# Kernel tuning notes

Measured on AMD Instinct MI355X. Metric: run time of the kernel, lower is better.

The kernel has to match this reference:

```python
import jax, jax.numpy as jnp
from jax import lax
import numpy as np

B, T = 512, 64
VOCAB, EMB, HID, NIMG = 10000, 512, 1024, 2048


def setup_inputs() -> dict:
    key = jax.random.key(0)
    ks = jax.random.split(key, 8)
    s_ih = 1.0 / np.sqrt(HID)
    return {
        "m": jax.random.randint(ks[0], (B, T), 0, VOCAB),
        "emb": jax.random.normal(ks[1], (VOCAB, EMB), dtype=jnp.float32),
        "W_ih": jax.random.uniform(ks[2], (4 * HID, EMB), minval=-s_ih, maxval=s_ih, dtype=jnp.float32),
        "W_hh": jax.random.uniform(ks[3], (4 * HID, HID), minval=-s_ih, maxval=s_ih, dtype=jnp.float32),
        "b_ih": jax.random.uniform(ks[4], (4 * HID,), minval=-s_ih, maxval=s_ih, dtype=jnp.float32),
        "b_hh": jax.random.uniform(ks[5], (4 * HID,), minval=-s_ih, maxval=s_ih, dtype=jnp.float32),
        "W_out": jax.random.normal(ks[6], (NIMG, HID), dtype=jnp.float32) * (1.0 / np.sqrt(HID)),
        "b_out": jnp.zeros((NIMG,), dtype=jnp.float32),
    }


def reference(m, emb, W_ih, W_hh, b_ih, b_hh, W_out, b_out):
    # m: [B, T] int tokens. Embed all steps at once, scan over time.
    x = emb[m]                      # [B, T, E]
    x = jnp.swapaxes(x, 0, 1)       # [T, B, E] (matches m.permute(1,0) step order)
    Bsz = m.shape[0]
    H = W_hh.shape[1]
    h0 = jnp.zeros((Bsz, H), dtype=emb.dtype)
    c0 = jnp.zeros((Bsz, H), dtype=emb.dtype)

    def step(carry, xt):
        h, c = carry
        # PyTorch LSTMCell gate order: input, forget, cell(g), output
        gates = xt @ W_ih.T + b_ih + h @ W_hh.T + b_hh  # [B, 4H]
        i, f, g, o = jnp.split(gates, 4, axis=-1)
        i = jax.nn.sigmoid(i)
        f = jax.nn.sigmoid(f)
        g = jnp.tanh(g)
        o = jax.nn.sigmoid(o)
        c = f * c + i * g
        h = o * jnp.tanh(c)
        return (h, c), None

    (h, _), _ = lax.scan(step, (h0, c0), x)
    return h @ W_out.T + b_out      # [B, n_image_features]
```

## Files before the change

kernel.cpp:

```cpp
#include <hip/hip_runtime.h>
#include <cstdint>

#define B_    512
#define T_    64
#define VOCAB_ 10000
#define VPAD_ 10112
#define EMB_  512
#define HID_  1024
#define G4H_  4096
#define KCAT_ 1536
#define NIMG_ 2048

typedef _Float16 half8 __attribute__((ext_vector_type(8)));
typedef _Float16 half4 __attribute__((ext_vector_type(4)));
typedef float floatx4 __attribute__((ext_vector_type(4)));

__device__ __forceinline__ void async_copy16(void* lds_uniform, const void* gsrc) {
    __builtin_amdgcn_global_load_lds(
        (__attribute__((address_space(1))) void*)(uintptr_t)gsrc,
        (__attribute__((address_space(3))) void*)(uint32_t)(uintptr_t)lds_uniform,
        16, 0, 0);
}

__device__ __forceinline__ float fsig(float x)  { return 1.0f / (1.0f + __expf(-x)); }
__device__ __forceinline__ float ftanh(float x) { return 1.0f - 2.0f / (__expf(2.0f * x) + 1.0f); }


__global__ __launch_bounds__(256) void convert_kernel(
    const int* __restrict__ m, const float* __restrict__ emb,
    const float* __restrict__ W_ih, const float* __restrict__ W_hh,
    const float* __restrict__ b_ih, const float* __restrict__ b_hh,
    const float* __restrict__ W_out,
    _Float16* __restrict__ emb16, _Float16* __restrict__ Wc16,
    _Float16* __restrict__ Wout16, float* __restrict__ biasp,
    _Float16* __restrict__ Hseq, int* __restrict__ tokperm)
{
    const long long EMB_N = (long long)VOCAB_ * EMB_;
    const long long WC_N  = (long long)G4H_ * KCAT_;
    const long long WO_N  = (long long)NIMG_ * HID_;
    const long long BI_N  = G4H_;
    const long long ST_N  = (long long)B_ * HID_;
    const long long TK_N  = (long long)B_ * T_;

    long long i = (long long)blockIdx.x * 256 + threadIdx.x;
    if (i < EMB_N) { emb16[i] = (_Float16)emb[i]; return; }
    i -= EMB_N;
    if (i < WC_N) {
        int n_perm = (int)(i / KCAT_);
        int k      = (int)(i % KCAT_);
        int gate = (n_perm >> 4) & 3;
        int j    = (n_perm >> 6) * 16 + (n_perm & 15);
        int n_orig = gate * HID_ + j;
        float v = (k < EMB_) ? W_ih[(size_t)n_orig * EMB_ + k]
                             : W_hh[(size_t)n_orig * HID_ + (k - EMB_)];
        Wc16[i] = (_Float16)v;
        return;
    }
    i -= WC_N;
    if (i < WO_N) { Wout16[i] = (_Float16)W_out[i]; return; }
    i -= WO_N;
    if (i < BI_N) {
        int n_perm = (int)i;
        int gate = (n_perm >> 4) & 3;
        int j    = (n_perm >> 6) * 16 + (n_perm & 15);
        biasp[i] = b_ih[gate * HID_ + j] + b_hh[gate * HID_ + j];
        return;
    }
    i -= BI_N;
    if (i < ST_N) { Hseq[i] = (_Float16)0.0f; return; }
    i -= ST_N;
    if (i < TK_N) {
        int t = (int)(i / B_), b = (int)(i % B_);
        tokperm[i] = m[(size_t)b * T_ + t];
    }
}

__global__ __launch_bounds__(256) void gemm_pe(
    const _Float16* __restrict__ emb16, const _Float16* __restrict__ Wc16,
    const float* __restrict__ biasp, _Float16* __restrict__ PEx)
{
    __shared__ __align__(16) _Float16 As[128 * 32];
    __shared__ __align__(16) _Float16 Bs[128 * 32];

    const int tid  = threadIdx.x;
    const int wid  = tid >> 6;
    const int lane = tid & 63;
    const int lcol = lane & 15;
    const int quad = lane >> 4;
    const int wm   = wid >> 1;
    const int wn   = wid & 1;

    const int r0 = blockIdx.x * 128;
    const int n0 = blockIdx.y * 128;

    floatx4 acc[4][4];
#pragma unroll
    for (int i = 0; i < 4; ++i)
#pragma unroll
        for (int j = 0; j < 4; ++j) acc[i][j] = (floatx4){0.f, 0.f, 0.f, 0.f};

    const int ar = tid >> 2;
    const int kq = tid & 3;

    for (int k0 = 0; k0 < EMB_; k0 += 32) {
        async_copy16((char*)As + (wid << 10),
                     emb16 + (size_t)(r0 + ar) * EMB_ + (k0 + kq * 8));
        async_copy16((char*)As + 4096 + (wid << 10),
                     emb16 + (size_t)(r0 + 64 + ar) * EMB_ + (k0 + kq * 8));
        async_copy16((char*)Bs + (wid << 10),
                     Wc16 + (size_t)(n0 + ar) * KCAT_ + (k0 + kq * 8));
        async_copy16((char*)Bs + 4096 + (wid << 10),
                     Wc16 + (size_t)(n0 + 64 + ar) * KCAT_ + (k0 + kq * 8));
        __syncthreads();

        half8 af[4], bf[4];
#pragma unroll
        for (int mi = 0; mi < 4; ++mi)
            af[mi] = *(const half8*)&As[(wm * 64 + mi * 16 + lcol) * 32 + quad * 8];
#pragma unroll
        for (int ni = 0; ni < 4; ++ni)
            bf[ni] = *(const half8*)&Bs[(wn * 64 + ni * 16 + lcol) * 32 + quad * 8];
#pragma unroll
        for (int mi = 0; mi < 4; ++mi)
#pragma unroll
            for (int ni = 0; ni < 4; ++ni)
                acc[mi][ni] = __builtin_amdgcn_mfma_f32_16x16x32_f16(
                    af[mi], bf[ni], acc[mi][ni], 0, 0, 0);
        __syncthreads();
    }

    const int jblk = (n0 + wn * 64) >> 6;
    float bv[4];
#pragma unroll
    for (int ni = 0; ni < 4; ++ni) bv[ni] = biasp[n0 + wn * 64 + ni * 16 + lcol];
#pragma unroll
    for (int mi = 0; mi < 4; ++mi) {
#pragma unroll
        for (int r = 0; r < 4; ++r) {
            const int row = r0 + wm * 64 + mi * 16 + quad * 4 + r;
            half4 v;
#pragma unroll
            for (int ni = 0; ni < 4; ++ni)
                v[ni] = (_Float16)(acc[mi][ni][r] + bv[ni]);
            *(half4*)(PEx + (size_t)row * G4H_ + jblk * 64 + lcol * 4) = v;
        }
    }
}

__global__ __launch_bounds__(256, 1) void lstm_persistent(
    const _Float16* __restrict__ PEx, const int* __restrict__ tokperm,
    const _Float16* __restrict__ Wc16,
    _Float16* __restrict__ Hseq,
    unsigned* __restrict__ flags)
{
    __shared__ __align__(16) char Wlds[131072];

    const int tid  = threadIdx.x;
    const int wid  = tid >> 6;
    const int lane = tid & 63;
    const int lcol = lane & 15;
    const int quad = lane >> 4;
    const int bx   = blockIdx.x;
    const int b0   = bx * 128;
    const int by   = blockIdx.y;
    const int n0   = by * 64;
    const int rot  = (by & 1) * 16;

    __builtin_amdgcn_fence(__ATOMIC_ACQUIRE, "agent");

    for (int si = 0; si < 8; ++si) {
        const int s = wid * 8 + si;
#pragma unroll
        for (int g = 0; g < 4; ++g) {
            half8 v = *(const half8*)(Wc16 + (size_t)(n0 + g * 16 + lcol) * KCAT_
                                      + EMB_ + s * 32 + quad * 8);
            *(half8*)(Wlds + (((s * 4 + g) << 6) + lane) * 16) = v;
        }
    }

    float cst[2][4] = {{0.f, 0.f, 0.f, 0.f}, {0.f, 0.f, 0.f, 0.f}};
    half4 pe[2][4];

#pragma unroll
    for (int mi = 0; mi < 2; ++mi)
#pragma unroll
        for (int r = 0; r < 4; ++r) {
            const int row = wid * 32 + mi * 16 + quad * 4 + r;
            const int tk = tokperm[b0 + row];
            pe[mi][r] = *(const half4*)(PEx + (size_t)tk * G4H_ + by * 64 + lcol * 4);
        }

    __syncthreads();

    const int wrow = wid * 32;
    const unsigned long long mA =
        rot ? 0xFFFFFFFF00000000ull : 0x00000000FFFFFFFFull;

    for (int t = 0; t < T_; ++t) {
        const _Float16* h_prev = Hseq + (size_t)t * (B_ * HID_);
        _Float16*       h_next = Hseq + (size_t)(t + 1) * (B_ * HID_);

        const unsigned want = 0x5AB00000u + (unsigned)(t - 1);
        const unsigned* f = flags + ((size_t)(t > 0 ? t - 1 : 0) * 4 + bx) * 64;

        unsigned long long rdy = (t == 0) ? ~0ull : 0ull;
        auto waitm = [&](unsigned long long need) {
            if ((rdy & need) == need) return;
            for (;;) {
                rdy = __ballot((int)(__hip_atomic_load(&f[lane], __ATOMIC_RELAXED,
                                                       __HIP_MEMORY_SCOPE_AGENT) == want));
                if ((rdy & need) == need) break;
                __builtin_amdgcn_s_sleep(1);
            }
            asm volatile("" ::: "memory");
        };

        const _Float16* arow0 = h_prev + (size_t)(b0 + wrow + lcol) * HID_ + quad * 8;
        const _Float16* arow1 = arow0 + (size_t)16 * HID_;

        floatx4 acc[2][4];
#pragma unroll
        for (int mi = 0; mi < 2; ++mi)
#pragma unroll
            for (int g = 0; g < 4; ++g)
#pragma unroll
                for (int r = 0; r < 4; ++r)
                    acc[mi][g][r] = (float)pe[mi][r][g];

        waitm(mA);
        half8 pa0[8], pa1[8];
#pragma unroll
        for (int c = 0; c < 8; ++c) {
            const int cs = (c + rot) & 31;
            pa0[c] = *(const half8*)(arow0 + cs * 32);
            pa1[c] = *(const half8*)(arow1 + cs * 32);
        }
        waitm(~mA);

#pragma unroll
        for (int s = 0; s < 32; ++s) {
            const int cs = (s + rot) & 31;
            const half8 a0 = pa0[s & 7];
            const half8 a1 = pa1[s & 7];
            if (s + 8 < 32) {
                const int cs8 = (s + 8 + rot) & 31;
                pa0[s & 7] = *(const half8*)(arow0 + cs8 * 32);
                pa1[s & 7] = *(const half8*)(arow1 + cs8 * 32);
            }
#pragma unroll
            for (int g = 0; g < 4; ++g) {
                const half8 bw = *(const half8*)(Wlds + (((cs * 4 + g) << 6) + lane) * 16);
                acc[0][g] = __builtin_amdgcn_mfma_f32_16x16x32_f16(a0, bw, acc[0][g], 0, 0, 0);
                acc[1][g] = __builtin_amdgcn_mfma_f32_16x16x32_f16(a1, bw, acc[1][g], 0, 0, 0);
            }
        }

#pragma unroll
        for (int mi = 0; mi < 2; ++mi)
#pragma unroll
            for (int r = 0; r < 4; ++r) {
                const int row = wrow + mi * 16 + quad * 4 + r;
                const float iv = fsig(acc[mi][0][r]);
                const float fv = fsig(acc[mi][1][r]);
                const float gv = ftanh(acc[mi][2][r]);
                const float ov = fsig(acc[mi][3][r]);
                cst[mi][r] = fv * cst[mi][r] + iv * gv;
                const _Float16 hv = (_Float16)(ov * ftanh(cst[mi][r]));
                unsigned short us = __builtin_bit_cast(unsigned short, hv);
                __hip_atomic_store(
                    (unsigned short*)&h_next[(size_t)(b0 + row) * HID_ + by * 16 + lcol],
                    us, __ATOMIC_RELAXED, __HIP_MEMORY_SCOPE_AGENT);
            }

        __syncthreads();
        if (tid == 0) {
            __hip_atomic_store(&flags[((size_t)t * 4 + bx) * 64 + by],
                               0x5AB00000u + (unsigned)t,
                               __ATOMIC_RELAXED, __HIP_MEMORY_SCOPE_AGENT);
        }

        if (t + 1 < T_) {
#pragma unroll
            for (int mi = 0; mi < 2; ++mi)
#pragma unroll
                for (int r = 0; r < 4; ++r) {
                    const int row = wrow + mi * 16 + quad * 4 + r;
                    const int tk = tokperm[(t + 1) * B_ + b0 + row];
                    pe[mi][r] = *(const half4*)(PEx + (size_t)tk * G4H_ + by * 64 + lcol * 4);
                }
        }
    }
}

__global__ __launch_bounds__(256) void gemm_out(
    const _Float16* __restrict__ A, const _Float16* __restrict__ Bw,
    const float* __restrict__ bias, float* __restrict__ Out, int N, int K)
{
    __shared__ __align__(16) _Float16 As[64 * 32];
    __shared__ __align__(16) _Float16 Bs[128 * 32];

    const int tid  = threadIdx.x;
    const int wid  = tid >> 6;
    const int lane = tid & 63;
    const int lcol = lane & 15;
    const int quad = lane >> 4;
    const int wm   = wid >> 1;
    const int wn   = wid & 1;

    const int b0 = blockIdx.x * 64;
    const int n0 = blockIdx.y * 128;

    floatx4 acc[2][4];
#pragma unroll
    for (int i = 0; i < 2; ++i)
#pragma unroll
        for (int j = 0; j < 4; ++j) acc[i][j] = (floatx4){0.f, 0.f, 0.f, 0.f};

    const int ar = tid >> 2;
    const int kq = tid & 3;

    for (int k0 = 0; k0 < K; k0 += 32) {
        async_copy16((char*)As + (wid << 10), A + (size_t)(b0 + ar) * K + (k0 + kq * 8));
        async_copy16((char*)Bs + (wid << 10), Bw + (size_t)(n0 + ar) * K + (k0 + kq * 8));
        async_copy16((char*)Bs + 4096 + (wid << 10),
                     Bw + (size_t)(n0 + 64 + ar) * K + (k0 + kq * 8));
        __syncthreads();

        half8 af[2], bfr[4];
#pragma unroll
        for (int mi = 0; mi < 2; ++mi)
            af[mi] = *(const half8*)&As[(wm * 32 + mi * 16 + lcol) * 32 + quad * 8];
#pragma unroll
        for (int ni = 0; ni < 4; ++ni)
            bfr[ni] = *(const half8*)&Bs[(wn * 64 + ni * 16 + lcol) * 32 + quad * 8];
#pragma unroll
        for (int mi = 0; mi < 2; ++mi)
#pragma unroll
            for (int ni = 0; ni < 4; ++ni)
                acc[mi][ni] = __builtin_amdgcn_mfma_f32_16x16x32_f16(
                    af[mi], bfr[ni], acc[mi][ni], 0, 0, 0);
        __syncthreads();
    }

#pragma unroll
    for (int mi = 0; mi < 2; ++mi) {
#pragma unroll
        for (int ni = 0; ni < 4; ++ni) {
            const int row = b0 + wm * 32 + mi * 16 + quad * 4;
            const int col = n0 + wn * 64 + ni * 16 + lcol;
            const float bv = bias[col];
#pragma unroll
            for (int r = 0; r < 4; ++r)
                Out[(size_t)(row + r) * N + col] = acc[mi][ni][r] + bv;
        }
    }
}

extern "C" void kernel_launch(void* const* d_in, const int* in_sizes, int n_in,
                              void* d_out, int out_size, void* d_ws, size_t ws_size,
                              hipStream_t stream)
{
    const int*   m     = (const int*)d_in[0];
    const float* emb   = (const float*)d_in[1];
    const float* W_ih  = (const float*)d_in[2];
    const float* W_hh  = (const float*)d_in[3];
    const float* b_ih  = (const float*)d_in[4];
    const float* b_hh  = (const float*)d_in[5];
    const float* W_out = (const float*)d_in[6];
    const float* b_out = (const float*)d_in[7];
    float* out = (float*)d_out;

    char* w = (char*)d_ws;
    size_t off = 0;
    auto alloc = [&](size_t bytes) {
        char* p = w + off;
        off = (off + bytes + 255) & ~(size_t)255;
        return p;
    };
    _Float16* emb16   = (_Float16*)alloc((size_t)VPAD_ * EMB_ * 2);
    _Float16* Wc16    = (_Float16*)alloc((size_t)G4H_ * KCAT_ * 2);
    _Float16* Wout16  = (_Float16*)alloc((size_t)NIMG_ * HID_ * 2);
    float*    biasp   = (float*)   alloc((size_t)G4H_ * 4);
    _Float16* Hseq    = (_Float16*)alloc((size_t)(T_ + 1) * B_ * HID_ * 2);
    int*      tokperm = (int*)     alloc((size_t)B_ * T_ * 4);
    unsigned* flags   = (unsigned*)alloc((size_t)T_ * 4 * 64 * 4);
    _Float16* PEx     = (_Float16*)alloc((size_t)VPAD_ * G4H_ * 2);

    {
        const long long total = (long long)VOCAB_ * EMB_ + (long long)G4H_ * KCAT_ +
                                (long long)NIMG_ * HID_ + G4H_ +
                                (long long)B_ * HID_ + (long long)B_ * T_;
        convert_kernel<<<(int)((total + 255) / 256), 256, 0, stream>>>(
            m, emb, W_ih, W_hh, b_ih, b_hh, W_out,
            emb16, Wc16, Wout16, biasp, Hseq, tokperm);
    }

    gemm_pe<<<dim3(VPAD_ / 128, G4H_ / 128), 256, 0, stream>>>(
        emb16, Wc16, biasp, PEx);

    lstm_persistent<<<dim3(B_ / 128, G4H_ / 64), 256, 0, stream>>>(
        PEx, tokperm, Wc16, Hseq, flags);

    gemm_out<<<dim3(B_ / 64, NIMG_ / 128), 256, 0, stream>>>(
        Hseq + (size_t)T_ * B_ * HID_, Wout16, b_out, out, NIMG_, HID_);
}
```

Baseline: 856.4 us.

## Split LSTM recurrence across twice as many blocks with narrower gate tiles

Halves each persistent block's gate slice from 64 to 32 columns, so the grid doubles to 512 blocks and each block needs only 64KB of LDS, which allows two blocks per CU. The weight and bias permutation is changed so 8 hidden units' four gates sit in one 32-column tile, and gates are exchanged across lanes with shuffles. The cross-block flag array and wait logic are widened to 128 producers per row group. This spreads the recurrent matmul over more CUs at the cost of more flag polling per step and half the lanes idling during the output store.

```diff
diff --git a/kernel.cpp b/kernel.cpp
--- a/kernel.cpp
+++ b/kernel.cpp
@@ -13,6 +13,7 @@
 
 typedef _Float16 half8 __attribute__((ext_vector_type(8)));
 typedef _Float16 half4 __attribute__((ext_vector_type(4)));
+typedef _Float16 half2v __attribute__((ext_vector_type(2)));
 typedef float floatx4 __attribute__((ext_vector_type(4)));
 
 __device__ __forceinline__ void async_copy16(void* lds_uniform, const void* gsrc) {
@@ -48,9 +49,10 @@
     if (i < WC_N) {
         int n_perm = (int)(i / KCAT_);
         int k      = (int)(i % KCAT_);
-        int gate = (n_perm >> 4) & 3;
-        int j    = (n_perm >> 6) * 16 + (n_perm & 15);
-        int n_orig = gate * HID_ + j;
+        int q    = n_perm >> 5;
+        int gate = (n_perm >> 3) & 3;
+        int u    = n_perm & 7;
+        int n_orig = gate * HID_ + q * 8 + u;
         float v = (k < EMB_) ? W_ih[(size_t)n_orig * EMB_ + k]
                              : W_hh[(size_t)n_orig * HID_ + (k - EMB_)];
         Wc16[i] = (_Float16)v;
@@ -61,9 +63,10 @@
     i -= WO_N;
     if (i < BI_N) {
         int n_perm = (int)i;
-        int gate = (n_perm >> 4) & 3;
-        int j    = (n_perm >> 6) * 16 + (n_perm & 15);
-        biasp[i] = b_ih[gate * HID_ + j] + b_hh[gate * HID_ + j];
+        int q    = n_perm >> 5;
+        int gate = (n_perm >> 3) & 3;
+        int u    = n_perm & 7;
+        biasp[i] = b_ih[gate * HID_ + q * 8 + u] + b_hh[gate * HID_ + q * 8 + u];
         return;
     }
     i -= BI_N;
@@ -129,7 +132,8 @@
         __syncthreads();
     }
 
-    const int jblk = (n0 + wn * 64) >> 6;
+    const int u   = lcol & 7;
+    const int pp0 = (lcol >= 8) ? 2 : 0;
     float bv[4];
 #pragma unroll
     for (int ni = 0; ni < 4; ++ni) bv[ni] = biasp[n0 + wn * 64 + ni * 16 + lcol];
@@ -138,22 +142,25 @@
 #pragma unroll
         for (int r = 0; r < 4; ++r) {
             const int row = r0 + wm * 64 + mi * 16 + quad * 4 + r;
-            half4 v;
-#pragma unroll
-            for (int ni = 0; ni < 4; ++ni)
-                v[ni] = (_Float16)(acc[mi][ni][r] + bv[ni]);
-            *(half4*)(PEx + (size_t)row * G4H_ + jblk * 64 + lcol * 4) = v;
-        }
-    }
-}
-
-__global__ __launch_bounds__(256, 1) void lstm_persistent(
+#pragma unroll
+            for (int nip = 0; nip < 2; ++nip) {
+                const int q = (n0 + wn * 64 + nip * 32) >> 5;
+                half2v v;
+                v[0] = (_Float16)(acc[mi][2 * nip][r]     + bv[2 * nip]);
+                v[1] = (_Float16)(acc[mi][2 * nip + 1][r] + bv[2 * nip + 1]);
+                *(half2v*)(PEx + (size_t)row * G4H_ + q * 32 + u * 4 + pp0) = v;
+            }
+        }
+    }
+}
+
+__global__ __launch_bounds__(256, 2) void lstm_persistent(
     const _Float16* __restrict__ PEx, const int* __restrict__ tokperm,
     const _Float16* __restrict__ Wc16,
     _Float16* __restrict__ Hseq,
     unsigned* __restrict__ flags)
 {
-    __shared__ __align__(16) char Wlds[131072];
+    __shared__ __align__(16) char Wlds[65536];
 
     const int tid  = threadIdx.x;
     const int wid  = tid >> 6;
@@ -163,23 +170,25 @@
     const int bx   = blockIdx.x;
     const int b0   = bx * 128;
     const int by   = blockIdx.y;
-    const int n0   = by * 64;
+    const int n0   = by * 32;
     const int rot  = (by & 1) * 16;
+    const int u    = lcol & 7;
+    const int pp0  = (lcol >= 8) ? 2 : 0;
 
     __builtin_amdgcn_fence(__ATOMIC_ACQUIRE, "agent");
 
     for (int si = 0; si < 8; ++si) {
         const int s = wid * 8 + si;
 #pragma unroll
-        for (int g = 0; g < 4; ++g) {
-            half8 v = *(const half8*)(Wc16 + (size_t)(n0 + g * 16 + lcol) * KCAT_
+        for (int ni = 0; ni < 2; ++ni) {
+            half8 v = *(const half8*)(Wc16 + (size_t)(n0 + ni * 16 + lcol) * KCAT_
                                       + EMB_ + s * 32 + quad * 8);
-            *(half8*)(Wlds + (((s * 4 + g) << 6) + lane) * 16) = v;
+            *(half8*)(Wlds + (((s * 2 + ni) << 6) + lane) * 16) = v;
         }
     }
 
     float cst[2][4] = {{0.f, 0.f, 0.f, 0.f}, {0.f, 0.f, 0.f, 0.f}};
-    half4 pe[2][4];
+    half2v pe[2][4];
 
 #pragma unroll
     for (int mi = 0; mi < 2; ++mi)
@@ -187,47 +196,42 @@
         for (int r = 0; r < 4; ++r) {
             const int row = wid * 32 + mi * 16 + quad * 4 + r;
             const int tk = tokperm[b0 + row];
-            pe[mi][r] = *(const half4*)(PEx + (size_t)tk * G4H_ + by * 64 + lcol * 4);
+            pe[mi][r] = *(const half2v*)(PEx + (size_t)tk * G4H_ + by * 32 + u * 4 + pp0);
         }
 
     __syncthreads();
 
     const int wrow = wid * 32;
-    const unsigned long long mA =
-        rot ? 0xFFFFFFFF00000000ull : 0x00000000FFFFFFFFull;
+    const int gA = rot >> 4;
 
     for (int t = 0; t < T_; ++t) {
         const _Float16* h_prev = Hseq + (size_t)t * (B_ * HID_);
         _Float16*       h_next = Hseq + (size_t)(t + 1) * (B_ * HID_);
 
         const unsigned want = 0x5AB00000u + (unsigned)(t - 1);
-        const unsigned* f = flags + ((size_t)(t > 0 ? t - 1 : 0) * 4 + bx) * 64;
-
-        unsigned long long rdy = (t == 0) ? ~0ull : 0ull;
-        auto waitm = [&](unsigned long long need) {
-            if ((rdy & need) == need) return;
-            for (;;) {
-                rdy = __ballot((int)(__hip_atomic_load(&f[lane], __ATOMIC_RELAXED,
-                                                       __HIP_MEMORY_SCOPE_AGENT) == want));
-                if ((rdy & need) == need) break;
+        const unsigned* f = flags + ((size_t)(t > 0 ? t - 1 : 0) * 4 + bx) * 128;
+
+        auto waitg = [&](int g) {
+            if (t == 0) return;
+            while (!__all((int)(__hip_atomic_load(&f[g * 64 + lane], __ATOMIC_RELAXED,
+                                                  __HIP_MEMORY_SCOPE_AGENT) == want)))
                 __builtin_amdgcn_s_sleep(1);
-            }
             asm volatile("" ::: "memory");
         };
 
         const _Float16* arow0 = h_prev + (size_t)(b0 + wrow + lcol) * HID_ + quad * 8;
         const _Float16* arow1 = arow0 + (size_t)16 * HID_;
 
-        floatx4 acc[2][4];
+        floatx4 acc[2][2];
 #pragma unroll
         for (int mi = 0; mi < 2; ++mi)
 #pragma unroll
-            for (int g = 0; g < 4; ++g)
-#pragma unroll
-                for (int r = 0; r < 4; ++r)
-                    acc[mi][g][r] = (float)pe[mi][r][g];
-
-        waitm(mA);
+            for (int r = 0; r < 4; ++r) {
+                acc[mi][0][r] = (float)pe[mi][r][0];
+                acc[mi][1][r] = (float)pe[mi][r][1];
+            }
+
+        waitg(gA);
         half8 pa0[8], pa1[8];
 #pragma unroll
         for (int c = 0; c < 8; ++c) {
@@ -235,7 +239,7 @@
             pa0[c] = *(const half8*)(arow0 + cs * 32);
             pa1[c] = *(const half8*)(arow1 + cs * 32);
         }
-        waitm(~mA);
+        waitg(1 - gA);
 
 #pragma unroll
         for (int s = 0; s < 32; ++s) {
@@ -247,34 +251,41 @@
                 pa0[s & 7] = *(const half8*)(arow0 + cs8 * 32);
                 pa1[s & 7] = *(const half8*)(arow1 + cs8 * 32);
             }
-#pragma unroll
-            for (int g = 0; g < 4; ++g) {
-                const half8 bw = *(const half8*)(Wlds + (((cs * 4 + g) << 6) + lane) * 16);
-                acc[0][g] = __builtin_amdgcn_mfma_f32_16x16x32_f16(a0, bw, acc[0][g], 0, 0, 0);
-                acc[1][g] = __builtin_amdgcn_mfma_f32_16x16x32_f16(a1, bw, acc[1][g], 0, 0, 0);
-            }
+            const half8 bw0 = *(const half8*)(Wlds + (((cs * 2 + 0) << 6) + lane) * 16);
+            const half8 bw1 = *(const half8*)(Wlds + (((cs * 2 + 1) << 6) + lane) * 16);
+            acc[0][0] = __builtin_amdgcn_mfma_f32_16x16x32_f16(a0, bw0, acc[0][0], 0, 0, 0);
+            acc[0][1] = __builtin_amdgcn_mfma_f32_16x16x32_f16(a0, bw1, acc[0][1], 0, 0, 0);
+            acc[1][0] = __builtin_amdgcn_mfma_f32_16x16x32_f16(a1, bw0, acc[1][0], 0, 0, 0);
+            acc[1][1] = __builtin_amdgcn_mfma_f32_16x16x32_f16(a1, bw1, acc[1][1], 0, 0, 0);
         }
 
 #pragma unroll
         for (int mi = 0; mi < 2; ++mi)
 #pragma unroll
             for (int r = 0; r < 4; ++r) {
-                const int row = wrow + mi * 16 + quad * 4 + r;
-                const float iv = fsig(acc[mi][0][r]);
-                const float fv = fsig(acc[mi][1][r]);
-                const float gv = ftanh(acc[mi][2][r]);
-                const float ov = fsig(acc[mi][3][r]);
+                const float own0 = acc[mi][0][r];
+                const float own1 = acc[mi][1][r];
+                const float oth0 = __shfl_xor(own0, 8);
+                const float oth1 = __shfl_xor(own1, 8);
+                const float iv = fsig((lcol < 8) ? own0 : oth0);
+                const float gv = ftanh((lcol < 8) ? own1 : oth1);
+                const float fv = fsig((lcol < 8) ? oth0 : own0);
+                const float ov = fsig((lcol < 8) ? oth1 : own1);
                 cst[mi][r] = fv * cst[mi][r] + iv * gv;
-                const _Float16 hv = (_Float16)(ov * ftanh(cst[mi][r]));
-                unsigned short us = __builtin_bit_cast(unsigned short, hv);
-                __hip_atomic_store(
-                    (unsigned short*)&h_next[(size_t)(b0 + row) * HID_ + by * 16 + lcol],
-                    us, __ATOMIC_RELAXED, __HIP_MEMORY_SCOPE_AGENT);
+                const float hval = ov * ftanh(cst[mi][r]);
+                if (lcol < 8) {
+                    const int row = wrow + mi * 16 + quad * 4 + r;
+                    const _Float16 hv = (_Float16)hval;
+                    unsigned short us = __builtin_bit_cast(unsigned short, hv);
+                    __hip_atomic_store(
+                        (unsigned short*)&h_next[(size_t)(b0 + row) * HID_ + by * 8 + u],
+                        us, __ATOMIC_RELAXED, __HIP_MEMORY_SCOPE_AGENT);
+                }
             }
 
         __syncthreads();
         if (tid == 0) {
-            __hip_atomic_store(&flags[((size_t)t * 4 + bx) * 64 + by],
+            __hip_atomic_store(&flags[((size_t)t * 4 + bx) * 128 + by],
                                0x5AB00000u + (unsigned)t,
                                __ATOMIC_RELAXED, __HIP_MEMORY_SCOPE_AGENT);
         }
@@ -286,7 +297,7 @@
                 for (int r = 0; r < 4; ++r) {
                     const int row = wrow + mi * 16 + quad * 4 + r;
                     const int tk = tokperm[(t + 1) * B_ + b0 + row];
-                    pe[mi][r] = *(const half4*)(PEx + (size_t)tk * G4H_ + by * 64 + lcol * 4);
+                    pe[mi][r] = *(const half2v*)(PEx + (size_t)tk * G4H_ + by * 32 + u * 4 + pp0);
                 }
         }
     }
@@ -383,7 +394,7 @@
     float*    biasp   = (float*)   alloc((size_t)G4H_ * 4);
     _Float16* Hseq    = (_Float16*)alloc((size_t)(T_ + 1) * B_ * HID_ * 2);
     int*      tokperm = (int*)     alloc((size_t)B_ * T_ * 4);
-    unsigned* flags   = (unsigned*)alloc((size_t)T_ * 4 * 64 * 4);
+    unsigned* flags   = (unsigned*)alloc((size_t)T_ * 4 * 128 * 4);
     _Float16* PEx     = (_Float16*)alloc((size_t)VPAD_ * G4H_ * 2);
 
     {
@@ -398,7 +409,7 @@
     gemm_pe<<<dim3(VPAD_ / 128, G4H_ / 128), 256, 0, stream>>>(
         emb16, Wc16, biasp, PEx);
 
-    lstm_persistent<<<dim3(B_ / 128, G4H_ / 64), 256, 0, stream>>>(
+    lstm_persistent<<<dim3(4, 128), 256, 0, stream>>>(
         PEx, tokperm, Wc16, Hseq, flags);
 
     gemm_out<<<dim3(B_ / 64, NIMG_ / 128), 256, 0, stream>>>(
```

New measurement: 1.568 ms. +83.1%, slower.
